# Kernel optimization log

Hardware: AMD Instinct MI355X
Metric: run time of the kernel (lower is better)

## Reference

```python
import jax, jax.numpy as jnp
import numpy as np

B, T, I, H, F1, C = 65536, 30, 26, 24, 8, 4  # batch, seq_len, input, hidden, fc1, classes


def setup_inputs() -> dict:
    key = jax.random.key(0)
    ks = jax.random.split(key, 9)
    s_ih = 1.0 / np.sqrt(H)
    return {
        "x": jax.random.normal(ks[0], (B, T, I), dtype=jnp.float32),
        "W_ih": jax.random.uniform(ks[1], (3 * H, I), jnp.float32, -s_ih, s_ih),
        "W_hh": jax.random.uniform(ks[2], (3 * H, H), jnp.float32, -s_ih, s_ih),
        "b_ih": jax.random.uniform(ks[3], (3 * H,), jnp.float32, -s_ih, s_ih),
        "b_hh": jax.random.uniform(ks[4], (3 * H,), jnp.float32, -s_ih, s_ih),
        "fc1_w": jax.random.normal(ks[5], (F1, H), jnp.float32) * 0.1,
        "fc1_b": jax.random.normal(ks[6], (F1,), jnp.float32) * 0.1,
        "fc2_w": jax.random.normal(ks[7], (C, F1), jnp.float32) * 0.1,
        "fc2_b": jax.random.normal(ks[8], (C,), jnp.float32) * 0.1,
    }


def reference(x, W_ih, W_hh, b_ih, b_hh, fc1_w, fc1_b, fc2_w, fc2_b):
    # Precompute input projections for all timesteps: (B, T, 3H)
    xp = jnp.einsum("bti,gi->btg", x, W_ih) + b_ih

    def step(h, xt):  # h: (B,H), xt: (B,3H)
        gh = h @ W_hh.T + b_hh  # (B, 3H)
        xr, xz, xn = jnp.split(xt, 3, axis=-1)
        hr, hz, hn = jnp.split(gh, 3, axis=-1)
        r = jax.nn.sigmoid(xr + hr)
        z = jax.nn.sigmoid(xz + hz)
        n = jnp.tanh(xn + r * hn)
        h_new = (1.0 - z) * n + z * h
        return h_new, None

    h0 = jnp.zeros((x.shape[0], W_hh.shape[1]), dtype=x.dtype)
    h, _ = jax.lax.scan(step, h0, jnp.swapaxes(xp, 0, 1))  # final hidden (B, H)

    # eval mode: dropout is identity
    hid = jax.nn.relu(h @ fc1_w.T + fc1_b)
    logits = hid @ fc2_w.T + fc2_b
    return jax.nn.softmax(logits, axis=1)
```

## Files before the change

kernel.cpp:

```cpp
#include <hip/hip_runtime.h>

typedef __bf16 bf16x8 __attribute__((ext_vector_type(8)));
typedef float f32x4 __attribute__((ext_vector_type(4)));
typedef float f32x2 __attribute__((ext_vector_type(2)));

#define T_SEQ 30
#define NIN 26
#define XPITCH 780
#define LOG2E 1.44269504088896340736f

__device__ __forceinline__ float sig2(float s) {
    return __builtin_amdgcn_rcpf(1.f + __builtin_amdgcn_exp2f(-s));
}

#define LOADC(BUF, c, half) do {                                              \
    const int rr_ = (c) / 15, tt_ = (c) % 15 + (half) * 15;                   \
    const float* sp_ = x + (size_t)(b0 + rr_) * XPITCH + tt_ * NIN;           \
    _Pragma("unroll") for (int q_ = 0; q_ < 13; ++q_)                         \
        BUF[q_] = *(const f32x2*)(sp_ + 2 * q_);                              \
} while (0)

#define WRITEC(BUF, c, half) do {                                             \
    const int rr_ = (c) / 15, tt_ = (c) % 15 + (half) * 15;                   \
    const int id_ = rr_ * 30 + tt_;                                           \
    const int ix_ = (id_ ^ ((rr_ >> 2) & 3)) << 3;                            \
    _Pragma("unroll") for (int kk_ = 0; kk_ < 3; ++kk_) {                     \
        bf16x8 wv_;                                                           \
        _Pragma("unroll") for (int q_ = 0; q_ < 4; ++q_) {                    \
            wv_[2 * q_]     = (__bf16)BUF[kk_ * 4 + q_].x;                    \
            wv_[2 * q_ + 1] = (__bf16)BUF[kk_ * 4 + q_].y;                    \
        }                                                                     \
        *(bf16x8*)&xmain[kk_ * 7680 + ix_] = wv_;                             \
    }                                                                         \
    xtail[id_ * 2]     = (__bf16)BUF[12].x;                                   \
    xtail[id_ * 2 + 1] = (__bf16)BUF[12].y;                                   \
} while (0)

__global__ __launch_bounds__(128, 2) void gru_kernel(
    const float* __restrict__ x, const float* __restrict__ W_ih,
    const float* __restrict__ W_hh, const float* __restrict__ b_ih,
    const float* __restrict__ b_hh, const float* __restrict__ fc1_w,
    const float* __restrict__ fc1_b, const float* __restrict__ fc2_w,
    const float* __restrict__ fc2_b, float* __restrict__ out)
{
    __shared__ __attribute__((aligned(16))) __bf16 xmain[23040];
    __shared__ __attribute__((aligned(8)))  __bf16 xtail[1920];
    __shared__ __attribute__((aligned(16))) __bf16 hbuf[1024];
    __shared__ float wbuf[236];

    const int tid = threadIdx.x;
    const int lane = tid & 63;
    const int wid = tid >> 6;
    const int m = lane & 15;
    const int kg = lane >> 4;
    const int w16 = wid << 4;
    const int b0 = blockIdx.x << 5;

    for (int i = tid; i < 236; i += 128) {
        float v;
        if (i < 192) v = fc1_w[i];
        else if (i < 200) v = fc1_b[i - 192];
        else if (i < 232) v = fc2_w[i - 200];
        else v = fc2_b[i - 232];
        wbuf[i] = v;
    }
    for (int i = tid; i < 1024; i += 128) hbuf[i] = (__bf16)0.f;

    bf16x8 bIh[6], bHh[6];
    float bx[6], bh[6];
    #pragma unroll
    for (int Tn = 0; Tn < 6; ++Tn) {
        const float sc = (Tn < 4) ? LOG2E : (2.f * LOG2E);
        const int np = Tn * 16 + m;
        const int gp = np >> 5;
        const int jh = np & 31;
        const bool vc = jh < 24;
        const int g = gp * 24 + jh;
        #pragma unroll
        for (int e = 0; e < 8; ++e) {
            const int k = kg * 8 + e;
            bIh[Tn][e] = (__bf16)((vc && k < 26) ? W_ih[g * 26 + k] * sc : 0.f);
            bHh[Tn][e] = (__bf16)((vc && k < 24) ? W_hh[g * 24 + k] * sc : 0.f);
        }
        bx[Tn] = vc ? b_ih[g] * sc : 0.f;
        bh[Tn] = vc ? b_hh[g] * sc : 0.f;
    }
    const float brz0 = bx[0] + bh[0], brz1 = bx[1] + bh[1];
    const float brz2 = bx[2] + bh[2], brz3 = bx[3] + bh[3];
    const float bnx0 = bx[4], bnh0 = bh[4], bnx1 = bx[5], bnh1 = bh[5];

    {
        f32x2 bufA[13], bufB[13];
        LOADC(bufA, tid, 0);
        #pragma unroll
        for (int j = 0; j < 4; ++j) {
            if (j < 3) {
                const int cn = tid + (j + 1) * 128;
                if (cn < 480) LOADC(bufB, cn, 0);
            }
            const int cc = tid + j * 128;
            if (cc < 480) WRITEC(bufA, cc, 0);
            if (j < 3) {
                #pragma unroll
                for (int q = 0; q < 13; ++q) bufA[q] = bufB[q];
            }
        }
    }
    __syncthreads();

    const int rowg = w16 + m;
    const int sxr = (rowg >> 2) & 3;
    const int rbase = rowg * 30;
    const int ra  = m * 32 + ((kg ^ (m >> 2)) << 3);
    const int wr0 = (kg * 4) * 32 + ((((m >> 3) ^ kg) & 3) << 3) + (m & 7);
    const int wr1 = (kg * 4) * 32 + (((2 ^ kg) & 3) << 3) + m;
    __bf16* hw = &hbuf[wid * 512];

    f32x4 hc0 = {0.f, 0.f, 0.f, 0.f}, hc1 = {0.f, 0.f, 0.f, 0.f};
    const f32x4 z4 = {0.f, 0.f, 0.f, 0.f};
    f32x2 bufS[13];

    #pragma unroll 1
    for (int t = 0; t < T_SEQ; ++t) {
        if (t >= 1 && t <= 8) {
            if (t & 1) {
                const int c = tid + (((t - 1) >> 1) << 7);
                if (c < 480) LOADC(bufS, c, 1);
            } else {
                const int c = tid + (((t - 2) >> 1) << 7);
                if (c < 480) WRITEC(bufS, c, 1);
            }
        }
        if (t == 9) __syncthreads();

        bf16x8 ax;
        {
            const int id = rbase + t;
            if (kg < 3) {
                ax = *(const bf16x8*)&xmain[kg * 7680 + ((id ^ sxr) << 3)];
            } else {
                bf16x8 zz = {};
                zz[0] = xtail[id * 2];
                zz[1] = xtail[id * 2 + 1];
                ax = zz;
            }
        }
        const bf16x8 ah = *(const bf16x8*)&hw[ra];

        {
            f32x4 xr = __builtin_amdgcn_mfma_f32_16x16x32_bf16(ax, bIh[0], z4, 0, 0, 0);
            f32x4 hr = __builtin_amdgcn_mfma_f32_16x16x32_bf16(ah, bHh[0], z4, 0, 0, 0);
            f32x4 xz = __builtin_amdgcn_mfma_f32_16x16x32_bf16(ax, bIh[2], z4, 0, 0, 0);
            f32x4 hz = __builtin_amdgcn_mfma_f32_16x16x32_bf16(ah, bHh[2], z4, 0, 0, 0);
            f32x4 xn = __builtin_amdgcn_mfma_f32_16x16x32_bf16(ax, bIh[4], z4, 0, 0, 0);
            f32x4 hn = __builtin_amdgcn_mfma_f32_16x16x32_bf16(ah, bHh[4], z4, 0, 0, 0);
            #pragma unroll
            for (int r = 0; r < 4; ++r) {
                const float rg = sig2(xr[r] + hr[r] + brz0);
                const float zg = sig2(xz[r] + hz[r] + brz2);
                const float ag = xn[r] + bnx0 + rg * (hn[r] + bnh0);
                const float ng = 2.f * sig2(ag) - 1.f;
                hc0[r] = ng + zg * (hc0[r] - ng);
            }
            #pragma unroll
            for (int r = 0; r < 4; ++r)
                hw[wr0 + r * 32] = (__bf16)hc0[r];
        }

        {
            f32x4 xr = __builtin_amdgcn_mfma_f32_16x16x32_bf16(ax, bIh[1], z4, 0, 0, 0);
            f32x4 hr = __builtin_amdgcn_mfma_f32_16x16x32_bf16(ah, bHh[1], z4, 0, 0, 0);
            f32x4 xz = __builtin_amdgcn_mfma_f32_16x16x32_bf16(ax, bIh[3], z4, 0, 0, 0);
            f32x4 hz = __builtin_amdgcn_mfma_f32_16x16x32_bf16(ah, bHh[3], z4, 0, 0, 0);
            f32x4 xn = __builtin_amdgcn_mfma_f32_16x16x32_bf16(ax, bIh[5], z4, 0, 0, 0);
            f32x4 hn = __builtin_amdgcn_mfma_f32_16x16x32_bf16(ah, bHh[5], z4, 0, 0, 0);
            #pragma unroll
            for (int r = 0; r < 4; ++r) {
                const float rg = sig2(xr[r] + hr[r] + brz1);
                const float zg = sig2(xz[r] + hz[r] + brz3);
                const float ag = xn[r] + bnx1 + rg * (hn[r] + bnh1);
                const float ng = 2.f * sig2(ag) - 1.f;
                hc1[r] = ng + zg * (hc1[r] - ng);
            }
            if (m < 8) {
                #pragma unroll
                for (int r = 0; r < 4; ++r)
                    hw[wr1 + r * 32] = (__bf16)hc1[r];
            }
        }
    }

    if (lane < 16) {
        const int row = lane;
        float hv[24];
        #pragma unroll
        for (int j = 0; j < 24; ++j)
            hv[j] = (float)hw[row * 32 + ((((j >> 3) ^ (row >> 2)) & 3) << 3) + (j & 7)];
        float lg[4] = {wbuf[232], wbuf[233], wbuf[234], wbuf[235]};
        #pragma unroll
        for (int o = 0; o < 8; ++o) {
            float s = wbuf[192 + o];
            #pragma unroll
            for (int j = 0; j < 24; ++j) s += wbuf[o * 24 + j] * hv[j];
            s = fmaxf(s, 0.f);
            #pragma unroll
            for (int c = 0; c < 4; ++c) lg[c] += wbuf[200 + c * 8 + o] * s;
        }
        const float mx = fmaxf(fmaxf(lg[0], lg[1]), fmaxf(lg[2], lg[3]));
        const float e0 = __expf(lg[0] - mx), e1 = __expf(lg[1] - mx);
        const float e2 = __expf(lg[2] - mx), e3 = __expf(lg[3] - mx);
        const float inv = __builtin_amdgcn_rcpf(e0 + e1 + e2 + e3);
        f32x4 pr = {e0 * inv, e1 * inv, e2 * inv, e3 * inv};
        *(f32x4*)&out[(size_t)(b0 + w16 + row) * 4] = pr;
    }
}

extern "C" void kernel_launch(void* const* d_in, const int* in_sizes, int n_in,
                              void* d_out, int out_size, void* d_ws, size_t ws_size,
                              hipStream_t stream) {
    const float* xx    = (const float*)d_in[0];
    const float* w_ih  = (const float*)d_in[1];
    const float* w_hh  = (const float*)d_in[2];
    const float* bih   = (const float*)d_in[3];
    const float* bhh   = (const float*)d_in[4];
    const float* f1w   = (const float*)d_in[5];
    const float* f1b   = (const float*)d_in[6];
    const float* f2w   = (const float*)d_in[7];
    const float* f2b   = (const float*)d_in[8];
    float* outp = (float*)d_out;

    dim3 grid(65536 / 32), block(128);
    gru_kernel<<<grid, block, 0, stream>>>(xx, w_ih, w_hh, bih, bhh, f1w, f1b, f2w, f2b, outp);
}
```

Before: 382.3 us.

## Stream x through double-buffered 4-step LDS windows, larger blocks

Replaces the full-sequence LDS staging of x (30 timesteps per row) with a double-buffered window holding four timesteps. The next window is loaded from global memory while the current one is computed, with one barrier per four steps. Blocks grow to 256 threads covering 64 rows, and the lower LDS footprint is meant to allow more resident blocks per CU. The aim is to hide global load latency and raise occupancy, at the cost of more frequent barriers and global loads spread through the recurrence.

After: 356.7 us. -6.7%, faster.

```diff
diff --git a/kernel.cpp b/kernel.cpp
--- a/kernel.cpp
+++ b/kernel.cpp
@@ -9,43 +9,79 @@
 #define XPITCH 780
 #define LOG2E 1.44269504088896340736f
 
+#define KGS 520
+#define TWS (4 * KGS)
+#define BUFS (4 * TWS)
+
 __device__ __forceinline__ float sig2(float s) {
     return __builtin_amdgcn_rcpf(1.f + __builtin_amdgcn_exp2f(-s));
 }
 
-#define LOADC(BUF, c, half) do {                                              \
-    const int rr_ = (c) / 15, tt_ = (c) % 15 + (half) * 15;                   \
-    const float* sp_ = x + (size_t)(b0 + rr_) * XPITCH + tt_ * NIN;           \
-    _Pragma("unroll") for (int q_ = 0; q_ < 13; ++q_)                         \
-        BUF[q_] = *(const f32x2*)(sp_ + 2 * q_);                              \
-} while (0)
-
-#define WRITEC(BUF, c, half) do {                                             \
-    const int rr_ = (c) / 15, tt_ = (c) % 15 + (half) * 15;                   \
-    const int id_ = rr_ * 30 + tt_;                                           \
-    const int ix_ = (id_ ^ ((rr_ >> 2) & 3)) << 3;                            \
+#define WSTORE(BSEL) do {                                                     \
+    const int base_ = (BSEL) * BUFS + twn * TWS + rr * 8;                     \
     _Pragma("unroll") for (int kk_ = 0; kk_ < 3; ++kk_) {                     \
         bf16x8 wv_;                                                           \
         _Pragma("unroll") for (int q_ = 0; q_ < 4; ++q_) {                    \
-            wv_[2 * q_]     = (__bf16)BUF[kk_ * 4 + q_].x;                    \
-            wv_[2 * q_ + 1] = (__bf16)BUF[kk_ * 4 + q_].y;                    \
-        }                                                                     \
-        *(bf16x8*)&xmain[kk_ * 7680 + ix_] = wv_;                             \
+            wv_[2 * q_]     = (__bf16)sb[kk_ * 4 + q_].x;                     \
+            wv_[2 * q_ + 1] = (__bf16)sb[kk_ * 4 + q_].y;                     \
+        }                                                                     \
+        *(bf16x8*)&xwin[base_ + kk_ * KGS] = wv_;                             \
     }                                                                         \
-    xtail[id_ * 2]     = (__bf16)BUF[12].x;                                   \
-    xtail[id_ * 2 + 1] = (__bf16)BUF[12].y;                                   \
+    bf16x8 tv_ = {};                                                          \
+    tv_[0] = (__bf16)sb[12].x; tv_[1] = (__bf16)sb[12].y;                     \
+    *(bf16x8*)&xwin[base_ + 3 * KGS] = tv_;                                   \
 } while (0)
 
-__global__ __launch_bounds__(128, 2) void gru_kernel(
+#define STEP(TT, BSEL) do {                                                   \
+    const bf16x8 ax = *(const bf16x8*)&xwin[(BSEL) * BUFS + (TT) * TWS + xoff]; \
+    const bf16x8 ah = *(const bf16x8*)&hw[ra];                                \
+    {                                          \
+        f32x4 xr = __builtin_amdgcn_mfma_f32_16x16x32_bf16(ax, bIh[0], z4, 0, 0, 0); \
+        f32x4 hr = __builtin_amdgcn_mfma_f32_16x16x32_bf16(ah, bHh[0], z4, 0, 0, 0); \
+        f32x4 xz = __builtin_amdgcn_mfma_f32_16x16x32_bf16(ax, bIh[2], z4, 0, 0, 0); \
+        f32x4 hz = __builtin_amdgcn_mfma_f32_16x16x32_bf16(ah, bHh[2], z4, 0, 0, 0); \
+        f32x4 xn = __builtin_amdgcn_mfma_f32_16x16x32_bf16(ax, bIh[4], z4, 0, 0, 0); \
+        f32x4 hn = __builtin_amdgcn_mfma_f32_16x16x32_bf16(ah, bHh[4], z4, 0, 0, 0); \
+        _Pragma("unroll") for (int r = 0; r < 4; ++r) {                       \
+            const float rg = sig2(xr[r] + hr[r] + brz0);                      \
+            const float zg = sig2(xz[r] + hz[r] + brz2);                      \
+            const float ag = xn[r] + bnx0 + rg * (hn[r] + bnh0);              \
+            const float ng = 2.f * sig2(ag) - 1.f;                            \
+            hc0[r] = ng + zg * (hc0[r] - ng);                                 \
+        }                                                                     \
+        _Pragma("unroll") for (int r = 0; r < 4; ++r)                         \
+            hw[wr0 + r * 32] = (__bf16)hc0[r];                                \
+    }                                                                         \
+    {                                          \
+        f32x4 xr = __builtin_amdgcn_mfma_f32_16x16x32_bf16(ax, bIh[1], z4, 0, 0, 0); \
+        f32x4 hr = __builtin_amdgcn_mfma_f32_16x16x32_bf16(ah, bHh[1], z4, 0, 0, 0); \
+        f32x4 xz = __builtin_amdgcn_mfma_f32_16x16x32_bf16(ax, bIh[3], z4, 0, 0, 0); \
+        f32x4 hz = __builtin_amdgcn_mfma_f32_16x16x32_bf16(ah, bHh[3], z4, 0, 0, 0); \
+        f32x4 xn = __builtin_amdgcn_mfma_f32_16x16x32_bf16(ax, bIh[5], z4, 0, 0, 0); \
+        f32x4 hn = __builtin_amdgcn_mfma_f32_16x16x32_bf16(ah, bHh[5], z4, 0, 0, 0); \
+        _Pragma("unroll") for (int r = 0; r < 4; ++r) {                       \
+            const float rg = sig2(xr[r] + hr[r] + brz1);                      \
+            const float zg = sig2(xz[r] + hz[r] + brz3);                      \
+            const float ag = xn[r] + bnx1 + rg * (hn[r] + bnh1);              \
+            const float ng = 2.f * sig2(ag) - 1.f;                            \
+            hc1[r] = ng + zg * (hc1[r] - ng);                                 \
+        }                                                                     \
+        if (m < 8) {                                                          \
+            _Pragma("unroll") for (int r = 0; r < 4; ++r)                     \
+                hw[wr1 + r * 32] = (__bf16)hc1[r];                            \
+        }                                                                     \
+    }                                                                         \
+} while (0)
+
+__global__ __launch_bounds__(256, 4) void gru_kernel(
     const float* __restrict__ x, const float* __restrict__ W_ih,
     const float* __restrict__ W_hh, const float* __restrict__ b_ih,
     const float* __restrict__ b_hh, const float* __restrict__ fc1_w,
     const float* __restrict__ fc1_b, const float* __restrict__ fc2_w,
     const float* __restrict__ fc2_b, float* __restrict__ out)
 {
-    __shared__ __attribute__((aligned(16))) __bf16 xmain[23040];
-    __shared__ __attribute__((aligned(8)))  __bf16 xtail[1920];
-    __shared__ __attribute__((aligned(16))) __bf16 hbuf[1024];
+    __shared__ __attribute__((aligned(16))) __bf16 xwin[2 * BUFS];
+    __shared__ __attribute__((aligned(16))) __bf16 hbuf[2048];
     __shared__ float wbuf[236];
 
     const int tid = threadIdx.x;
@@ -54,17 +90,17 @@
     const int m = lane & 15;
     const int kg = lane >> 4;
     const int w16 = wid << 4;
-    const int b0 = blockIdx.x << 5;
-
-    for (int i = tid; i < 236; i += 128) {
+    const int b0 = blockIdx.x << 6;
+
+    if (tid < 236) {
         float v;
-        if (i < 192) v = fc1_w[i];
-        else if (i < 200) v = fc1_b[i - 192];
-        else if (i < 232) v = fc2_w[i - 200];
-        else v = fc2_b[i - 232];
-        wbuf[i] = v;
-    }
-    for (int i = tid; i < 1024; i += 128) hbuf[i] = (__bf16)0.f;
+        if (tid < 192) v = fc1_w[tid];
+        else if (tid < 200) v = fc1_b[tid - 192];
+        else if (tid < 232) v = fc2_w[tid - 200];
+        else v = fc2_b[tid - 232];
+        wbuf[tid] = v;
+    }
+    for (int i = tid; i < 2048; i += 256) hbuf[i] = (__bf16)0.f;
 
     bf16x8 bIh[6], bHh[6];
     float bx[6], bh[6];
@@ -89,28 +125,19 @@
     const float brz2 = bx[2] + bh[2], brz3 = bx[3] + bh[3];
     const float bnx0 = bx[4], bnh0 = bh[4], bnx1 = bx[5], bnh1 = bh[5];
 
+    const int rr = tid >> 2, twn = tid & 3;
+    const float* xrow = x + (size_t)(b0 + rr) * XPITCH;
+    f32x2 sb[13];
+
     {
-        f32x2 bufA[13], bufB[13];
-        LOADC(bufA, tid, 0);
-        #pragma unroll
-        for (int j = 0; j < 4; ++j) {
-            if (j < 3) {
-                const int cn = tid + (j + 1) * 128;
-                if (cn < 480) LOADC(bufB, cn, 0);
-            }
-            const int cc = tid + j * 128;
-            if (cc < 480) WRITEC(bufA, cc, 0);
-            if (j < 3) {
-                #pragma unroll
-                for (int q = 0; q < 13; ++q) bufA[q] = bufB[q];
-            }
-        }
+        const float* sp = xrow + twn * NIN;
+        #pragma unroll
+        for (int q = 0; q < 13; ++q) sb[q] = *(const f32x2*)(sp + 2 * q);
+        WSTORE(0);
     }
     __syncthreads();
 
-    const int rowg = w16 + m;
-    const int sxr = (rowg >> 2) & 3;
-    const int rbase = rowg * 30;
+    const int xoff = kg * KGS + (w16 + m) * 8;
     const int ra  = m * 32 + ((kg ^ (m >> 2)) << 3);
     const int wr0 = (kg * 4) * 32 + ((((m >> 3) ^ kg) & 3) << 3) + (m & 7);
     const int wr1 = (kg * 4) * 32 + (((2 ^ kg) & 3) << 3) + m;
@@ -118,77 +145,26 @@
 
     f32x4 hc0 = {0.f, 0.f, 0.f, 0.f}, hc1 = {0.f, 0.f, 0.f, 0.f};
     const f32x4 z4 = {0.f, 0.f, 0.f, 0.f};
-    f32x2 bufS[13];
 
     #pragma unroll 1
-    for (int t = 0; t < T_SEQ; ++t) {
-        if (t >= 1 && t <= 8) {
-            if (t & 1) {
-                const int c = tid + (((t - 1) >> 1) << 7);
-                if (c < 480) LOADC(bufS, c, 1);
-            } else {
-                const int c = tid + (((t - 2) >> 1) << 7);
-                if (c < 480) WRITEC(bufS, c, 1);
-            }
+    for (int w = 0; w < 7; ++w) {
+        {
+            const int tl0 = 4 * (w + 1) + twn;
+            const int tl = (tl0 > 29) ? 29 : tl0;
+            const float* sp = xrow + tl * NIN;
+            #pragma unroll
+            for (int q = 0; q < 13; ++q) sb[q] = *(const f32x2*)(sp + 2 * q);
         }
-        if (t == 9) __syncthreads();
-
-        bf16x8 ax;
-        {
-            const int id = rbase + t;
-            if (kg < 3) {
-                ax = *(const bf16x8*)&xmain[kg * 7680 + ((id ^ sxr) << 3)];
-            } else {
-                bf16x8 zz = {};
-                zz[0] = xtail[id * 2];
-                zz[1] = xtail[id * 2 + 1];
-                ax = zz;
-            }
-        }
-        const bf16x8 ah = *(const bf16x8*)&hw[ra];
-
-        {
-            f32x4 xr = __builtin_amdgcn_mfma_f32_16x16x32_bf16(ax, bIh[0], z4, 0, 0, 0);
-            f32x4 hr = __builtin_amdgcn_mfma_f32_16x16x32_bf16(ah, bHh[0], z4, 0, 0, 0);
-            f32x4 xz = __builtin_amdgcn_mfma_f32_16x16x32_bf16(ax, bIh[2], z4, 0, 0, 0);
-            f32x4 hz = __builtin_amdgcn_mfma_f32_16x16x32_bf16(ah, bHh[2], z4, 0, 0, 0);
-            f32x4 xn = __builtin_amdgcn_mfma_f32_16x16x32_bf16(ax, bIh[4], z4, 0, 0, 0);
-            f32x4 hn = __builtin_amdgcn_mfma_f32_16x16x32_bf16(ah, bHh[4], z4, 0, 0, 0);
-            #pragma unroll
-            for (int r = 0; r < 4; ++r) {
-                const float rg = sig2(xr[r] + hr[r] + brz0);
-                const float zg = sig2(xz[r] + hz[r] + brz2);
-                const float ag = xn[r] + bnx0 + rg * (hn[r] + bnh0);
-                const float ng = 2.f * sig2(ag) - 1.f;
-                hc0[r] = ng + zg * (hc0[r] - ng);
-            }
-            #pragma unroll
-            for (int r = 0; r < 4; ++r)
-                hw[wr0 + r * 32] = (__bf16)hc0[r];
-        }
-
-        {
-            f32x4 xr = __builtin_amdgcn_mfma_f32_16x16x32_bf16(ax, bIh[1], z4, 0, 0, 0);
-            f32x4 hr = __builtin_amdgcn_mfma_f32_16x16x32_bf16(ah, bHh[1], z4, 0, 0, 0);
-            f32x4 xz = __builtin_amdgcn_mfma_f32_16x16x32_bf16(ax, bIh[3], z4, 0, 0, 0);
-            f32x4 hz = __builtin_amdgcn_mfma_f32_16x16x32_bf16(ah, bHh[3], z4, 0, 0, 0);
-            f32x4 xn = __builtin_amdgcn_mfma_f32_16x16x32_bf16(ax, bIh[5], z4, 0, 0, 0);
-            f32x4 hn = __builtin_amdgcn_mfma_f32_16x16x32_bf16(ah, bHh[5], z4, 0, 0, 0);
-            #pragma unroll
-            for (int r = 0; r < 4; ++r) {
-                const float rg = sig2(xr[r] + hr[r] + brz1);
-                const float zg = sig2(xz[r] + hz[r] + brz3);
-                const float ag = xn[r] + bnx1 + rg * (hn[r] + bnh1);
-                const float ng = 2.f * sig2(ag) - 1.f;
-                hc1[r] = ng + zg * (hc1[r] - ng);
-            }
-            if (m < 8) {
-                #pragma unroll
-                for (int r = 0; r < 4; ++r)
-                    hw[wr1 + r * 32] = (__bf16)hc1[r];
-            }
-        }
-    }
+        const int bs = w & 1;
+        STEP(0, bs);
+        STEP(1, bs);
+        WSTORE(bs ^ 1);
+        STEP(2, bs);
+        STEP(3, bs);
+        __syncthreads();
+    }
+    STEP(0, 1);
+    STEP(1, 1);
 
     if (lane < 16) {
         const int row = lane;
@@ -229,6 +205,6 @@
     const float* f2b   = (const float*)d_in[8];
     float* outp = (float*)d_out;
 
-    dim3 grid(65536 / 32), block(128);
+    dim3 grid(65536 / 64), block(256);
     gru_kernel<<<grid, block, 0, stream>>>(xx, w_ih, w_hh, bih, bhh, f1w, f1b, f2w, f2b, outp);
 }
```
